# Kernel optimization log

Hardware: AMD Instinct MI355X
Metric: run time of the kernel (lower is better)

## Reference

```python
import jax, jax.numpy as jnp
import numpy as np

N_NODES = 100000
IN_CH = 128
HIDDEN = 256
N_EDGES = 500000


def setup_inputs() -> dict:
    key = jax.random.key(0)
    k1, k2, k3, k4, k5, k6 = jax.random.split(key, 6)
    latent_space = jax.random.normal(k1, (N_NODES, IN_CH), dtype=jnp.float32)
    edge_index = jax.random.randint(k2, (2, N_EDGES), 0, N_NODES, dtype=jnp.int64)
    # torch Linear params: W is [out, in], y = x @ W.T + b
    lim1 = 1.0 / np.sqrt(2 * IN_CH)
    W1 = jax.random.uniform(k3, (HIDDEN, 2 * IN_CH), minval=-lim1, maxval=lim1, dtype=jnp.float32)
    b1 = jax.random.uniform(k4, (HIDDEN,), minval=-lim1, maxval=lim1, dtype=jnp.float32)
    lim2 = 1.0 / np.sqrt(HIDDEN)
    W2 = jax.random.uniform(k5, (1, HIDDEN), minval=-lim2, maxval=lim2, dtype=jnp.float32)
    b2 = jax.random.uniform(k6, (1,), minval=-lim2, maxval=lim2, dtype=jnp.float32)
    return {"latent_space": latent_space, "W1": W1, "b1": b1, "W2": W2, "b2": b2,
            "edge_index": edge_index}


def reference(latent_space, W1, b1, W2, b2, edge_index):
    src, dst = edge_index[0], edge_index[1]
    h_src = latent_space[src]                      # [E, C]
    h_dst = latent_space[dst]                      # [E, C]
    h_pair = jnp.concatenate([h_src, h_dst], axis=1)  # [E, 2C]
    h = jax.nn.relu(h_pair @ W1.T + b1)            # [E, H]; dropout=0 (eval)
    logits = (h @ W2.T + b2).squeeze(-1)           # [E]
    return jax.nn.sigmoid(logits)
```

## Files before the change

### kernel.cpp

```cpp
#include <hip/hip_runtime.h>
#include <hip/hip_bf16.h>
#include <stdint.h>

#define M_NODES 100000
#define E_EDGES 500000
#define NCOL    512
#define HID     256

typedef unsigned short u16;
typedef u16   u16x8 __attribute__((ext_vector_type(8)));
typedef u16   u16x4 __attribute__((ext_vector_type(4)));
typedef __bf16 bf16x8 __attribute__((ext_vector_type(8)));
typedef float f32x4 __attribute__((ext_vector_type(4)));

static __device__ __forceinline__ u16 f2bf(float f) {
  uint32_t u = __float_as_uint(f);
  u += 0x7fff + ((u >> 16) & 1);
  return (u16)(u >> 16);
}
static __device__ __forceinline__ float bf2f(u16 h) {
  return __uint_as_float(((uint32_t)h) << 16);
}

#define GLOAD_LDS16(g, lds)                                                          \
  __builtin_amdgcn_global_load_lds(                                                  \
      (const __attribute__((address_space(1))) uint32_t*)(g),                        \
      (__attribute__((address_space(3))) uint32_t*)(lds), 16, 0, 0)

__global__ __launch_bounds__(256) void k_convert(const float* __restrict__ in,
                                                 u16* __restrict__ out, int n4) {
  int i = blockIdx.x * blockDim.x + threadIdx.x;
  int stride = gridDim.x * blockDim.x;
  for (; i < n4; i += stride) {
    float4 f = reinterpret_cast<const float4*>(in)[i];
    u16x4 o;
    o[0] = f2bf(f.x); o[1] = f2bf(f.y); o[2] = f2bf(f.z); o[3] = f2bf(f.w);
    reinterpret_cast<u16x4*>(out)[i] = o;
  }
}

__global__ __launch_bounds__(256) void k_weights(const float* __restrict__ W1,
                                                 u16* __restrict__ Bt) {
  int idx = blockIdx.x * 256 + threadIdx.x;
  int j = idx >> 7, kk = idx & 127;
  int s = kk >> 3, i = kk & 7;
  int ls = s ^ (j & 7);
  int k = ls * 8 + i;
  float w = (j < HID) ? W1[j * 256 + k] : W1[(j - HID) * 256 + 128 + k];
  Bt[idx] = f2bf(w);
}

__global__ __launch_bounds__(256, 2) void k_gemm(const u16* __restrict__ A,
                                                 const u16* __restrict__ Bt,
                                                 const float* __restrict__ b1,
                                                 u16* __restrict__ UV) {
  __shared__ __align__(16) u16 ldsA[128 * 128];
  __shared__ __align__(16) u16 ldsB[128 * 128];
  const int t = threadIdx.x;
  const int bm = blockIdx.x, bn = blockIdx.y;
  const int w = t >> 6, l = t & 63;

  {
    const int lr4 = l >> 4;
    const int ls  = l & 15;
    #pragma unroll
    for (int c = 0; c < 8; ++c) {
      const int chunk = w * 8 + c;
      const int row   = chunk * 4 + lr4;
      int grow = bm * 128 + row;
      if (grow >= M_NODES) grow = M_NODES - 1;
      const int gslot = ls ^ (row & 7);
      GLOAD_LDS16(A + (size_t)grow * 128 + gslot * 8, &ldsA[chunk * 512]);
      GLOAD_LDS16(Bt + (size_t)bn * 16384 + chunk * 512 + l * 8, &ldsB[chunk * 512]);
    }
  }
  __syncthreads();

  const int wm = (w >> 1) * 64;
  const int wn = (w & 1) * 64;
  const int lr = l & 15;
  const int lk = l >> 4;

  f32x4 acc[4][4];
  #pragma unroll
  for (int i = 0; i < 4; ++i)
    #pragma unroll
    for (int j = 0; j < 4; ++j) acc[i][j] = f32x4{0.f, 0.f, 0.f, 0.f};

  #pragma unroll
  for (int kk = 0; kk < 128; kk += 32) {
    const int s = (kk >> 3) + lk;
    bf16x8 fa[4], fb[4];
    #pragma unroll
    for (int mt = 0; mt < 4; ++mt) {
      int row = wm + mt * 16 + lr;
      fa[mt] = *reinterpret_cast<const bf16x8*>(&ldsA[row * 128 + ((s ^ (row & 7)) * 8)]);
    }
    #pragma unroll
    for (int nt = 0; nt < 4; ++nt) {
      int row = wn + nt * 16 + lr;
      fb[nt] = *reinterpret_cast<const bf16x8*>(&ldsB[row * 128 + ((s ^ (row & 7)) * 8)]);
    }
    #pragma unroll
    for (int nt = 0; nt < 4; ++nt)
      #pragma unroll
      for (int mt = 0; mt < 4; ++mt)
        acc[nt][mt] = __builtin_amdgcn_mfma_f32_16x16x32_bf16(fb[nt], fa[mt], acc[nt][mt], 0, 0, 0);
  }

  #pragma unroll
  for (int nt = 0; nt < 4; ++nt) {
    #pragma unroll
    for (int mt = 0; mt < 4; ++mt) {
      int mg = bm * 128 + wm + mt * 16 + lr;
      int ng = bn * 128 + wn + nt * 16 + lk * 4;
      if (mg < M_NODES) {
        u16x4 o;
        #pragma unroll
        for (int r = 0; r < 4; ++r) {
          float v = acc[nt][mt][r];
          int col = ng + r;
          if (col < HID) v += b1[col];
          o[r] = f2bf(v);
        }
        *reinterpret_cast<u16x4*>(&UV[(size_t)mg * NCOL + ng]) = o;
      }
    }
  }
}

__global__ __launch_bounds__(256, 8) void k_edge(const u16* __restrict__ UV,
                                                 const int* __restrict__ src,
                                                 const int* __restrict__ dst,
                                                 const float* __restrict__ W2,
                                                 const float* __restrict__ b2p,
                                                 float* __restrict__ out) {
  const int t = threadIdx.x;
  const int l = t & 63;
  const int sub = l & 15;
  const int eg = l >> 4;
  const int wid = blockIdx.x * 4 + (t >> 6);
  const int nw = gridDim.x * 4;

  float w2r[16];
  #pragma unroll
  for (int i = 0; i < 16; ++i) w2r[i] = W2[sub * 16 + i];
  const float b2 = *b2p;

  for (int e = wid * 4; e < E_EDGES; e += nw * 4) {
    const int s = src[e + eg];
    const int d = dst[e + eg];
    const u16* pu = UV + (size_t)s * NCOL + sub * 16;
    const u16* pv = UV + (size_t)d * NCOL + HID + sub * 16;
    u16x8 ua = *reinterpret_cast<const u16x8*>(pu);
    u16x8 ub = *reinterpret_cast<const u16x8*>(pu + 8);
    u16x8 va = *reinterpret_cast<const u16x8*>(pv);
    u16x8 vb = *reinterpret_cast<const u16x8*>(pv + 8);
    float a = 0.f;
    #pragma unroll
    for (int i = 0; i < 8; ++i) {
      float h = bf2f(ua[i]) + bf2f(va[i]);
      h = fmaxf(h, 0.f);
      a = fmaf(h, w2r[i], a);
    }
    #pragma unroll
    for (int i = 0; i < 8; ++i) {
      float h = bf2f(ub[i]) + bf2f(vb[i]);
      h = fmaxf(h, 0.f);
      a = fmaf(h, w2r[8 + i], a);
    }
    a += __shfl_xor(a, 1, 64);
    a += __shfl_xor(a, 2, 64);
    a += __shfl_xor(a, 4, 64);
    a += __shfl_xor(a, 8, 64);
    if (sub == 0) {
      out[e + eg] = 1.0f / (1.0f + __expf(-(a + b2)));
    }
  }
}

extern "C" void kernel_launch(void* const* d_in, const int* in_sizes, int n_in,
                              void* d_out, int out_size, void* d_ws, size_t ws_size,
                              hipStream_t stream) {
  const float* latent = (const float*)d_in[0];
  const float* W1     = (const float*)d_in[1];
  const float* b1     = (const float*)d_in[2];
  const float* W2     = (const float*)d_in[3];
  const float* b2     = (const float*)d_in[4];
  const int*   eidx   = (const int*)d_in[5];

  char* ws = (char*)d_ws;
  u16* latent_bf = (u16*)ws;
  u16* Btw       = (u16*)(ws + 25600000);
  u16* UV        = (u16*)(ws + 25600000 + 131072);

  k_convert<<<2048, 256, 0, stream>>>(latent, latent_bf, (M_NODES * 128) / 4);
  k_weights<<<256, 256, 0, stream>>>(W1, Btw);
  dim3 gg((M_NODES + 127) / 128, NCOL / 128);
  k_gemm<<<gg, 256, 0, stream>>>(latent_bf, Btw, b1, UV);
  k_edge<<<2048, 256, 0, stream>>>(UV, eidx, eidx + E_EDGES, W2, b2, (float*)d_out);
}
```

Measured before the change: 233.2 us.

## Fuse fp32-to-bf16 conversion into GEMM and keep weight fragments in registers

```diff
diff --git a/kernel.cpp b/kernel.cpp
--- a/kernel.cpp
+++ b/kernel.cpp
@@ -22,64 +22,53 @@
   return __uint_as_float(((uint32_t)h) << 16);
 }
 
-#define GLOAD_LDS16(g, lds)                                                          \
-  __builtin_amdgcn_global_load_lds(                                                  \
-      (const __attribute__((address_space(1))) uint32_t*)(g),                        \
-      (__attribute__((address_space(3))) uint32_t*)(lds), 16, 0, 0)
-
-__global__ __launch_bounds__(256) void k_convert(const float* __restrict__ in,
-                                                 u16* __restrict__ out, int n4) {
-  int i = blockIdx.x * blockDim.x + threadIdx.x;
-  int stride = gridDim.x * blockDim.x;
-  for (; i < n4; i += stride) {
-    float4 f = reinterpret_cast<const float4*>(in)[i];
-    u16x4 o;
-    o[0] = f2bf(f.x); o[1] = f2bf(f.y); o[2] = f2bf(f.z); o[3] = f2bf(f.w);
-    reinterpret_cast<u16x4*>(out)[i] = o;
-  }
-}
-
 __global__ __launch_bounds__(256) void k_weights(const float* __restrict__ W1,
                                                  u16* __restrict__ Bt) {
   int idx = blockIdx.x * 256 + threadIdx.x;
-  int j = idx >> 7, kk = idx & 127;
-  int s = kk >> 3, i = kk & 7;
-  int ls = s ^ (j & 7);
-  int k = ls * 8 + i;
+  int j = idx >> 7, k = idx & 127;
   float w = (j < HID) ? W1[j * 256 + k] : W1[(j - HID) * 256 + 128 + k];
   Bt[idx] = f2bf(w);
 }
 
-__global__ __launch_bounds__(256, 2) void k_gemm(const u16* __restrict__ A,
+__global__ __launch_bounds__(512, 2) void k_gemm(const float* __restrict__ latent,
                                                  const u16* __restrict__ Bt,
                                                  const float* __restrict__ b1,
                                                  u16* __restrict__ UV) {
-  __shared__ __align__(16) u16 ldsA[128 * 128];
-  __shared__ __align__(16) u16 ldsB[128 * 128];
-  const int t = threadIdx.x;
-  const int bm = blockIdx.x, bn = blockIdx.y;
-  const int w = t >> 6, l = t & 63;
+  __shared__ __align__(16) u16 ldsA[64 * 128];
+  const int t  = threadIdx.x;
+  const int w  = t >> 6;
+  const int l  = t & 63;
+  const int lr = l & 15;
+  const int lk = l >> 4;
+  const int bm = blockIdx.x;
+
+  bf16x8 fb[4][4];
+  {
+    const u16* bp = Bt + ((size_t)(w * 64 + lr)) * 128 + lk * 8;
+    #pragma unroll
+    for (int nt = 0; nt < 4; ++nt)
+      #pragma unroll
+      for (int ks = 0; ks < 4; ++ks)
+        fb[nt][ks] = *reinterpret_cast<const bf16x8*>(bp + nt * 16 * 128 + ks * 32);
+  }
 
   {
-    const int lr4 = l >> 4;
-    const int ls  = l & 15;
+    const float4* lat4 = reinterpret_cast<const float4*>(latent);
     #pragma unroll
-    for (int c = 0; c < 8; ++c) {
-      const int chunk = w * 8 + c;
-      const int row   = chunk * 4 + lr4;
-      int grow = bm * 128 + row;
+    for (int i = 0; i < 4; ++i) {
+      int idx = i * 512 + t;
+      int row = idx >> 5;
+      int c4  = idx & 31;
+      int grow = bm * 64 + row;
       if (grow >= M_NODES) grow = M_NODES - 1;
-      const int gslot = ls ^ (row & 7);
-      GLOAD_LDS16(A + (size_t)grow * 128 + gslot * 8, &ldsA[chunk * 512]);
-      GLOAD_LDS16(Bt + (size_t)bn * 16384 + chunk * 512 + l * 8, &ldsB[chunk * 512]);
+      float4 f = lat4[(size_t)grow * 32 + c4];
+      u16x4 o;
+      o[0] = f2bf(f.x); o[1] = f2bf(f.y); o[2] = f2bf(f.z); o[3] = f2bf(f.w);
+      int ss = (c4 >> 1) ^ (row & 7);
+      *reinterpret_cast<u16x4*>(&ldsA[row * 128 + ss * 8 + (c4 & 1) * 4]) = o;
     }
   }
   __syncthreads();
-
-  const int wm = (w >> 1) * 64;
-  const int wn = (w & 1) * 64;
-  const int lr = l & 15;
-  const int lk = l >> 4;
 
   f32x4 acc[4][4];
   #pragma unroll
@@ -88,41 +77,36 @@
     for (int j = 0; j < 4; ++j) acc[i][j] = f32x4{0.f, 0.f, 0.f, 0.f};
 
   #pragma unroll
-  for (int kk = 0; kk < 128; kk += 32) {
-    const int s = (kk >> 3) + lk;
-    bf16x8 fa[4], fb[4];
+  for (int ks = 0; ks < 4; ++ks) {
+    bf16x8 fa[4];
     #pragma unroll
     for (int mt = 0; mt < 4; ++mt) {
-      int row = wm + mt * 16 + lr;
-      fa[mt] = *reinterpret_cast<const bf16x8*>(&ldsA[row * 128 + ((s ^ (row & 7)) * 8)]);
-    }
-    #pragma unroll
-    for (int nt = 0; nt < 4; ++nt) {
-      int row = wn + nt * 16 + lr;
-      fb[nt] = *reinterpret_cast<const bf16x8*>(&ldsB[row * 128 + ((s ^ (row & 7)) * 8)]);
+      int row = mt * 16 + lr;
+      int ss  = ((4 * ks + lk) ^ (row & 7));
+      fa[mt] = *reinterpret_cast<const bf16x8*>(&ldsA[row * 128 + ss * 8]);
     }
     #pragma unroll
     for (int nt = 0; nt < 4; ++nt)
       #pragma unroll
       for (int mt = 0; mt < 4; ++mt)
-        acc[nt][mt] = __builtin_amdgcn_mfma_f32_16x16x32_bf16(fb[nt], fa[mt], acc[nt][mt], 0, 0, 0);
+        acc[nt][mt] = __builtin_amdgcn_mfma_f32_16x16x32_bf16(fb[nt][ks], fa[mt], acc[nt][mt], 0, 0, 0);
   }
 
   #pragma unroll
   for (int nt = 0; nt < 4; ++nt) {
+    const int ng = w * 64 + nt * 16 + lk * 4;
+    float b1v[4] = {0.f, 0.f, 0.f, 0.f};
+    if (ng < HID) {
+      #pragma unroll
+      for (int r = 0; r < 4; ++r) b1v[r] = b1[ng + r];
+    }
     #pragma unroll
     for (int mt = 0; mt < 4; ++mt) {
-      int mg = bm * 128 + wm + mt * 16 + lr;
-      int ng = bn * 128 + wn + nt * 16 + lk * 4;
+      int mg = bm * 64 + mt * 16 + lr;
       if (mg < M_NODES) {
         u16x4 o;
         #pragma unroll
-        for (int r = 0; r < 4; ++r) {
-          float v = acc[nt][mt][r];
-          int col = ng + r;
-          if (col < HID) v += b1[col];
-          o[r] = f2bf(v);
-        }
+        for (int r = 0; r < 4; ++r) o[r] = f2bf(acc[nt][mt][r] + b1v[r]);
         *reinterpret_cast<u16x4*>(&UV[(size_t)mg * NCOL + ng]) = o;
       }
     }
@@ -190,13 +174,10 @@
   const int*   eidx   = (const int*)d_in[5];
 
   char* ws = (char*)d_ws;
-  u16* latent_bf = (u16*)ws;
-  u16* Btw       = (u16*)(ws + 25600000);
-  u16* UV        = (u16*)(ws + 25600000 + 131072);
+  u16* Btw = (u16*)ws;
+  u16* UV  = (u16*)(ws + 131072);
 
-  k_convert<<<2048, 256, 0, stream>>>(latent, latent_bf, (M_NODES * 128) / 4);
   k_weights<<<256, 256, 0, stream>>>(W1, Btw);
-  dim3 gg((M_NODES + 127) / 128, NCOL / 128);
-  k_gemm<<<gg, 256, 0, stream>>>(latent_bf, Btw, b1, UV);
+  k_gemm<<<(M_NODES + 63) / 64, 512, 0, stream>>>(latent, Btw, b1, UV);
   k_edge<<<2048, 256, 0, stream>>>(UV, eidx, eidx + E_EDGES, W2, b2, (float*)d_out);
 }
```

After: 228.7 us. No clear change (-1.9%).
